# Kernel tuning notes

Measured on AMD Instinct MI355X. Metric: run time of the kernel, lower is better.

The kernel has to match this reference:

```python
import jax, jax.numpy as jnp
import numpy as np

N_NODES = 100000
N_EDGES = 1600000
N_PAIRS = 500000
K_HOPS = 6


def _bn(x, g, b, eps):
    # training-mode batch norm over the node/edge (batch) axis, biased variance
    mu = jnp.mean(x, axis=0)
    var = jnp.var(x, axis=0)
    return (x - mu) * jax.lax.rsqrt(var + eps) * g + b


def _gelu(x):
    return jax.nn.gelu(x, approximate=False)  # torch GELU default (erf)


def setup_inputs() -> dict:
    key = jax.random.key(0)
    ks = jax.random.split(key, 20)
    F, EF = 128, 32

    def w(k, shape, s=0.05):
        return jax.random.normal(k, shape, dtype=jnp.float32) * s

    return {
        'X': jax.random.normal(ks[0], (N_NODES, F), jnp.float32),
        'Y': jax.random.normal(ks[1], (N_PAIRS, EF), jnp.float32),
        'edge_index': jax.random.randint(ks[2], (2, N_EDGES), 0, N_NODES, jnp.int32),
        'inds0': jax.random.randint(ks[3], (N_PAIRS,), 0, N_NODES, jnp.int32),
        'inds1': jax.random.randint(ks[4], (N_PAIRS,), 0, N_NODES, jnp.int32),
        'bn_node_g': jnp.ones((F,), jnp.float32),
        'bn_node_b': jnp.zeros((F,), jnp.float32),
        'tag_lin_W': w(ks[5], (F, 128)),
        'tag_lin_b': jnp.zeros((128,), jnp.float32),
        'tag_Ws': w(ks[6], (K_HOPS + 1, 128, 128)),
        'tag_bias': jnp.zeros((128,), jnp.float32),
        'nl_W0': w(ks[7], (256, 256)),
        'nl_b0': jnp.zeros((256,), jnp.float32),
        'nl_W1': w(ks[8], (256, 128)),
        'nl_b1': jnp.zeros((128,), jnp.float32),
        'cl_W': w(ks[9], (128, 128)),
        'cl_b': jnp.zeros((128,), jnp.float32),
        'end_W': w(ks[10], (128, 8)),
        'end_b': jnp.zeros((8,), jnp.float32),
        'bn_edge_g': jnp.ones((544,), jnp.float32),
        'bn_edge_b': jnp.zeros((544,), jnp.float32),
        'el_W0': w(ks[11], (544, 512)),
        'el_b0': jnp.zeros((512,), jnp.float32),
        'el_W1': w(ks[12], (512, 256)),
        'el_b1': jnp.zeros((256,), jnp.float32),
        'el_end_W': w(ks[13], (256, 1)),
        'el_end_b': jnp.zeros((1,), jnp.float32),
    }


def reference(X, Y, bn_node_g, bn_node_b, tag_lin_W, tag_lin_b, tag_Ws, tag_bias,
              nl_W0, nl_b0, nl_W1, nl_b1, cl_W, cl_b, end_W, end_b,
              bn_edge_g, bn_edge_b, el_W0, el_b0, el_W1, el_b1, el_end_W, el_end_b,
              edge_index, inds0, inds1):
    N = X.shape[0]
    # ---- NodeGLAM ----
    x = _bn(X, bn_node_g, bn_node_b, 1e-5)
    # TagModule: Linear -> GELU -> TAGConv -> GELU
    h = _gelu(x @ tag_lin_W + tag_lin_b)
    src, dst = edge_index[0], edge_index[1]
    # gcn_norm (no self loops): deg over target, norm = d^-1/2[src]*d^-1/2[dst]
    deg = jax.ops.segment_sum(jnp.ones(src.shape, h.dtype), dst, num_segments=N)
    dinv = jnp.where(deg > 0, jax.lax.rsqrt(jnp.maximum(deg, 1.0)), 0.0)
    wgt = (dinv[src] * dinv[dst])[:, None]  # [E,1]
    out = h @ tag_Ws[0]
    hk = h
    for k in range(1, K_HOPS + 1):
        hk = jax.ops.segment_sum(hk[src] * wgt, dst, num_segments=N)  # gather-scale-scatter
        out = out + hk @ tag_Ws[k]
    h = _gelu(out + tag_bias)
    a = jnp.concatenate([x, h], axis=1)  # [N, 256]
    a = _gelu(a @ nl_W0 + nl_b0)
    a = _gelu(a @ nl_W1 + nl_b1)  # Node_embs [N,128]
    cl = _gelu(a @ cl_W + cl_b)
    node_classes = jax.nn.softmax(cl @ end_W + end_b, axis=-1)  # [N,8]
    # ---- edge feature gather + EdgeGLAM ----
    Omega = jnp.concatenate([a[inds0], a[inds1], X[inds0], X[inds1], Y], axis=1)  # [P,544]
    o = _bn(Omega, bn_edge_g, bn_edge_b, 1.0)  # BatchNorm(input_, output_) -> eps=1
    o = _gelu(o @ el_W0 + el_b0)
    o = _gelu(o @ el_W1 + el_b1)
    e_pred = jax.nn.sigmoid(o @ el_end_W + el_end_b)[:, 0]  # [P]
    return (node_classes, e_pred)
```

## Files before the change

kernel.cpp:

```cpp
#include <hip/hip_runtime.h>
#include <math.h>

#define NN 100000
#define NE 1600000
#define NP 500000
#define KHOPS 6
#define ECHK 75000
#define NB_SCAN ((NN + 1023) / 1024)

typedef unsigned short u16;
typedef short bf16x8 __attribute__((ext_vector_type(8)));
typedef float f32x4 __attribute__((ext_vector_type(4)));

__device__ __forceinline__ float gelu_erf(float x) {
    return 0.5f * x * (1.0f + erff(x * 0.70710678118654752f));
}
__device__ __forceinline__ float b2f(u16 u) {
    return __uint_as_float(((unsigned int)u) << 16);
}
__device__ __forceinline__ u16 f2b(float f) {
    unsigned int x = __float_as_uint(f);
    return (u16)((x + 0x7FFFu + ((x >> 16) & 1u)) >> 16);
}
__device__ __forceinline__ bf16x8 cvt8(float4 a, float4 b) {
    bf16x8 v;
    v[0]=(short)f2b(a.x); v[1]=(short)f2b(a.y); v[2]=(short)f2b(a.z); v[3]=(short)f2b(a.w);
    v[4]=(short)f2b(b.x); v[5]=(short)f2b(b.y); v[6]=(short)f2b(b.z); v[7]=(short)f2b(b.w);
    return v;
}

template<int BF>
__global__ void col_stats(const void* __restrict__ Matv, int rows, int lc,
                          const int* __restrict__ w0, const int* __restrict__ w1,
                          float* __restrict__ sums, float* __restrict__ sumsq,
                          int base0, int base1)
{
    __shared__ float red[256];
    const int t = threadIdx.x;
    const int C = 1 << lc;
    const long total = (long)rows << lc;
    const long stride = (long)gridDim.x * 256;
    float s0 = 0.f, q0 = 0.f, s1 = 0.f, q1 = 0.f;
    for (long idx = (long)blockIdx.x * 256 + t; idx < total; idx += stride) {
        int r = (int)(idx >> lc);
        float v = BF ? b2f(((const u16*)Matv)[idx]) : ((const float*)Matv)[idx];
        float f0 = w0 ? (float)w0[r] : 1.0f;
        s0 += f0 * v;
        q0 += f0 * v * v;
        if (w1) {
            float f1 = (float)w1[r];
            s1 += f1 * v;
            q1 += f1 * v * v;
        }
    }
    red[t] = s0; __syncthreads();
    if (t < C) { float x = 0.f; for (int k = t; k < 256; k += C) x += red[k]; atomicAdd(&sums[base0 + t], x); }
    __syncthreads();
    red[t] = q0; __syncthreads();
    if (t < C) { float x = 0.f; for (int k = t; k < 256; k += C) x += red[k]; atomicAdd(&sumsq[base0 + t], x); }
    __syncthreads();
    if (w1) {
        red[t] = s1; __syncthreads();
        if (t < C) { float x = 0.f; for (int k = t; k < 256; k += C) x += red[k]; atomicAdd(&sums[base1 + t], x); }
        __syncthreads();
        red[t] = q1; __syncthreads();
        if (t < C) { float x = 0.f; for (int k = t; k < 256; k += C) x += red[k]; atomicAdd(&sumsq[base1 + t], x); }
    }
}

__global__ void bn_finalize(const float* __restrict__ sums, const float* __restrict__ sumsq,
                            const float* __restrict__ g, const float* __restrict__ b,
                            float* __restrict__ s, float* __restrict__ t,
                            int C, float count, float eps)
{
    int c = blockIdx.x * blockDim.x + threadIdx.x;
    if (c < C) {
        float mu = sums[c] / count;
        float var = sumsq[c] / count - mu * mu;
        float sc = g[c] * rsqrtf(var + eps);
        s[c] = sc;
        t[c] = b[c] - mu * sc;
    }
}

__global__ void gelu_bias_bf(const float* __restrict__ x, const float* __restrict__ bias,
                             u16* __restrict__ out, int n4)
{
    int stride = gridDim.x * blockDim.x;
    for (int i = blockIdx.x * blockDim.x + threadIdx.x; i < n4; i += stride) {
        int c4 = (i & 31) * 4;
        float4 v = ((const float4*)x)[i];
        ushort4 o;
        o.x = f2b(gelu_erf(v.x + bias[c4 + 0]));
        o.y = f2b(gelu_erf(v.y + bias[c4 + 1]));
        o.z = f2b(gelu_erf(v.z + bias[c4 + 2]));
        o.w = f2b(gelu_erf(v.w + bias[c4 + 3]));
        ((ushort4*)out)[i] = o;
    }
}

__global__ void hist_add(const int* __restrict__ idx, int n, int* __restrict__ cnt)
{
    int stride = gridDim.x * blockDim.x;
    for (int i = blockIdx.x * blockDim.x + threadIdx.x; i < n; i += stride)
        atomicAdd(&cnt[idx[i]], 1);
}

__global__ void hist_add2(const int* __restrict__ i0, const int* __restrict__ i1, int n,
                          int* __restrict__ c0, int* __restrict__ c1)
{
    int stride = gridDim.x * blockDim.x;
    for (int i = blockIdx.x * blockDim.x + threadIdx.x; i < n; i += stride) {
        atomicAdd(&c0[i0[i]], 1);
        atomicAdd(&c1[i1[i]], 1);
    }
}

__global__ void scan1(const int* __restrict__ cnt, int* __restrict__ ex,
                      int* __restrict__ part, int n)
{
    __shared__ int buf[1024];
    int b = blockIdx.x, t = threadIdx.x;
    int i = b * 1024 + t;
    int v = (i < n) ? cnt[i] : 0;
    buf[t] = v;
    __syncthreads();
    int incl = v;
    for (int o = 1; o < 1024; o <<= 1) {
        int tmp = (t >= o) ? buf[t - o] : 0;
        __syncthreads();
        incl += tmp;
        buf[t] = incl;
        __syncthreads();
    }
    if (i < n) ex[i] = incl - v;
    if (t == 1023) part[b] = incl;
}

__global__ void scan2(int* __restrict__ part, int nb)
{
    __shared__ int s[256];
    int t = threadIdx.x;
    if (t < nb) s[t] = part[t];
    __syncthreads();
    if (t == 0) {
        int run = 0;
        for (int b = 0; b < nb; ++b) { int x = s[b]; part[b] = run; run += x; }
        part[nb] = run;
    }
}

__global__ void scan3(int* __restrict__ indptr, const int* __restrict__ part,
                      const int* __restrict__ cnt, float* __restrict__ dinv, int n)
{
    int b = blockIdx.x, t = threadIdx.x;
    int i = b * 1024 + t;
    if (i < n) {
        indptr[i] += part[b];
        int c = cnt[i];
        dinv[i] = (c > 0) ? rsqrtf((float)c) : 0.f;
    }
    if (b == 0 && t == 0) indptr[n] = part[NB_SCAN];
}

__global__ void csr_build(const int* __restrict__ src, const int* __restrict__ dst, int n,
                          const int* __restrict__ indptr, int* __restrict__ cursor,
                          int* __restrict__ csrS)
{
    int stride = gridDim.x * blockDim.x;
    for (int e = blockIdx.x * blockDim.x + threadIdx.x; e < n; e += stride) {
        int s = src[e], d = dst[e];
        int pos = indptr[d] + atomicAdd(&cursor[d], 1);
        __builtin_nontemporal_store(s, &csrS[pos]);
    }
}

__global__ void spmm_hop(const u16* __restrict__ hin, u16* __restrict__ hout,
                         const int* __restrict__ indptr, const int* __restrict__ csrS,
                         const float* __restrict__ dinv)
{
    int gid = blockIdx.x * blockDim.x + threadIdx.x;
    int node = gid >> 6;
    int lane = gid & 63;
    if (node >= NN) return;
    float dn = dinv[node];
    int beg = indptr[node], end = indptr[node + 1];
    float a0 = 0.f, a1 = 0.f;
    int e = beg;
    for (; e + 1 < end; e += 2) {
        int s0 = csrS[e], s1 = csrS[e + 1];
        float w0 = dn * dinv[s0], w1 = dn * dinv[s1];
        ushort2 p0 = *(const ushort2*)(hin + (size_t)s0 * 128 + lane * 2);
        ushort2 p1 = *(const ushort2*)(hin + (size_t)s1 * 128 + lane * 2);
        a0 = fmaf(w0, b2f(p0.x), a0);
        a1 = fmaf(w0, b2f(p0.y), a1);
        a0 = fmaf(w1, b2f(p1.x), a0);
        a1 = fmaf(w1, b2f(p1.y), a1);
    }
    if (e < end) {
        int s0 = csrS[e];
        float w0 = dn * dinv[s0];
        ushort2 p0 = *(const ushort2*)(hin + (size_t)s0 * 128 + lane * 2);
        a0 = fmaf(w0, b2f(p0.x), a0);
        a1 = fmaf(w0, b2f(p0.y), a1);
    }
    ushort2 o;
    o.x = f2b(a0); o.y = f2b(a1);
    *(ushort2*)(hout + (size_t)node * 128 + lane * 2) = o;
}

__global__ void convTB(const float* __restrict__ in, u16* __restrict__ out,
                       int K, int Nc, int B)
{
    int per = K * Nc;
    int i = blockIdx.x * blockDim.x + threadIdx.x;
    if (i < per * B) {
        int m = i / per, r = i - m * per;
        int n = r / K, k = r - n * K;
        out[i] = f2b(in[(size_t)m * per + (size_t)k * Nc + n]);
    }
}

__global__ void fold_wT(const float* __restrict__ W0, const float* __restrict__ s,
                        u16* __restrict__ out)
{
    int i = blockIdx.x * blockDim.x + threadIdx.x;
    if (i < 512 * 544) {
        int n = i / 544, k = i - n * 544;
        out[i] = f2b(s[k] * W0[(size_t)k * 512 + n]);
    }
}

__global__ void fold_b(const float* __restrict__ W0, const float* __restrict__ b0,
                       const float* __restrict__ tv, float* __restrict__ bp)
{
    int j = blockIdx.x * blockDim.x + threadIdx.x;
    if (j < 512) {
        float s = b0[j];
        for (int k = 0; k < 544; ++k) s = fmaf(tv[k], W0[k * 512 + j], s);
        bp[j] = s;
    }
}

template<int AMODE>
__device__ __forceinline__ bf16x8 load_a_slot(
    const void* __restrict__ A0v, const void* __restrict__ A1v,
    const float* __restrict__ Yp, const int* __restrict__ i0s, const int* __restrict__ i1s,
    int rowOffset, const float* __restrict__ sv, const float* __restrict__ tv,
    int row, int r, int k0, int sl, int Mr, int lda)
{
    bf16x8 val = {0, 0, 0, 0, 0, 0, 0, 0};
    if (row < Mr) {
        if (AMODE == 0) {
            val = *(const bf16x8*)((const u16*)A0v + (size_t)row * lda + k0 + sl * 8);
        } else if (AMODE == 1) {
            int c = k0 + sl * 8;
            if (c < 128) {
                const float* xp = (const float*)A0v + (size_t)row * 128 + c;
                float4 x0 = *(const float4*)xp, x1 = *(const float4*)(xp + 4);
                float4 s0 = *(const float4*)(sv + c), s1 = *(const float4*)(sv + c + 4);
                float4 t0 = *(const float4*)(tv + c), t1 = *(const float4*)(tv + c + 4);
                float4 a = make_float4(fmaf(x0.x,s0.x,t0.x), fmaf(x0.y,s0.y,t0.y),
                                       fmaf(x0.z,s0.z,t0.z), fmaf(x0.w,s0.w,t0.w));
                float4 b = make_float4(fmaf(x1.x,s1.x,t1.x), fmaf(x1.y,s1.y,t1.y),
                                       fmaf(x1.z,s1.z,t1.z), fmaf(x1.w,s1.w,t1.w));
                val = cvt8(a, b);
            } else {
                val = *(const bf16x8*)((const u16*)A1v + (size_t)row * 128 + (c - 128));
            }
        } else if (AMODE == 3) {
            int c = k0 + sl * 8;
            const float* xp = (const float*)A0v + (size_t)row * 128 + c;
            float4 x0 = *(const float4*)xp, x1 = *(const float4*)(xp + 4);
            float4 s0 = *(const float4*)(sv + c), s1 = *(const float4*)(sv + c + 4);
            float4 t0 = *(const float4*)(tv + c), t1 = *(const float4*)(tv + c + 4);
            float4 a = make_float4(fmaf(x0.x,s0.x,t0.x), fmaf(x0.y,s0.y,t0.y),
                                   fmaf(x0.z,s0.z,t0.z), fmaf(x0.w,s0.w,t0.w));
            float4 b = make_float4(fmaf(x1.x,s1.x,t1.x), fmaf(x1.y,s1.y,t1.y),
                                   fmaf(x1.z,s1.z,t1.z), fmaf(x1.w,s1.w,t1.w));
            val = cvt8(a, b);
        } else {
            int seg = k0 >> 7;
            int c = (k0 & 127) + sl * 8;
            if (seg == 0) {
                val = *(const bf16x8*)((const u16*)A0v + (size_t)i0s[r] * 128 + c);
            } else if (seg == 1) {
                val = *(const bf16x8*)((const u16*)A0v + (size_t)i1s[r] * 128 + c);
            } else if (seg == 2) {
                const float* xp = (const float*)A1v + (size_t)i0s[r] * 128 + c;
                val = cvt8(*(const float4*)xp, *(const float4*)(xp + 4));
            } else if (seg == 3) {
                const float* xp = (const float*)A1v + (size_t)i1s[r] * 128 + c;
                val = cvt8(*(const float4*)xp, *(const float4*)(xp + 4));
            } else {
                const float* yp = Yp + (size_t)(rowOffset + row) * 32 + sl * 8;
                val = cvt8(*(const float4*)yp, *(const float4*)(yp + 4));
            }
        }
    }
    return val;
}

template<int AMODE, int ACT, int ACCUM, int OUTBF>
__launch_bounds__(256, 2)
__global__ void gemm_mfma(const void* __restrict__ A0v, const void* __restrict__ A1v,
                          const float* __restrict__ Yp,
                          const int* __restrict__ I0, const int* __restrict__ I1,
                          int rowOffset,
                          const float* __restrict__ sv, const float* __restrict__ tv,
                          const u16* __restrict__ Wb, const float* __restrict__ bias,
                          void* __restrict__ Cv, int Mr, int Kd, int Nc, int lda)
{
    __shared__ __align__(16) u16 As[128 * 32];
    __shared__ __align__(16) u16 Bs[128 * 32];
    __shared__ int i0s[128], i1s[128];

    const int t = threadIdx.x;
    const int lane = t & 63;
    const int wid = t >> 6;
    const int wm = wid >> 1, wn = wid & 1;
    const int lb = lane & 15, lh = lane >> 4;
    const int row0 = blockIdx.x * 128;
    const int colb = blockIdx.y * 128;

    if (AMODE == 2) {
        if (t < 128) {
            int r = row0 + t;
            i0s[t] = (r < Mr) ? I0[rowOffset + r] : 0;
        } else {
            int r = row0 + (t - 128);
            i1s[t - 128] = (r < Mr) ? I1[rowOffset + r] : 0;
        }
    }

    f32x4 acc[4][4];
#pragma unroll
    for (int i = 0; i < 4; ++i)
#pragma unroll
        for (int j = 0; j < 4; ++j) acc[i][j] = (f32x4){0.f, 0.f, 0.f, 0.f};

    for (int k0 = 0; k0 < Kd; k0 += 32) {
        __syncthreads();
#pragma unroll
        for (int h = 0; h < 2; ++h) {
            int s = t + h * 256;
            int r = s >> 2, sl = s & 3;
            bf16x8 val = load_a_slot<AMODE>(A0v, A1v, Yp, i0s, i1s, rowOffset, sv, tv,
                                            row0 + r, r, k0, sl, Mr, lda);
            *(bf16x8*)&As[r * 32 + ((sl ^ ((r >> 1) & 3)) << 3)] = val;
        }
#pragma unroll
        for (int h = 0; h < 2; ++h) {
            int s = t + h * 256;
            int n = s >> 2, sl = s & 3;
            bf16x8 val = *(const bf16x8*)(Wb + (size_t)(colb + n) * Kd + k0 + sl * 8);
            *(bf16x8*)&Bs[n * 32 + ((sl ^ ((n >> 1) & 3)) << 3)] = val;
        }
        __syncthreads();
        bf16x8 af[4], bfr[4];
#pragma unroll
        for (int i = 0; i < 4; ++i) {
            int r = wm * 64 + i * 16 + lb;
            af[i] = *(const bf16x8*)&As[r * 32 + ((lh ^ ((r >> 1) & 3)) << 3)];
        }
#pragma unroll
        for (int j = 0; j < 4; ++j) {
            int n = wn * 64 + j * 16 + lb;
            bfr[j] = *(const bf16x8*)&Bs[n * 32 + ((lh ^ ((n >> 1) & 3)) << 3)];
        }
#pragma unroll
        for (int i = 0; i < 4; ++i)
#pragma unroll
            for (int j = 0; j < 4; ++j)
                acc[i][j] = __builtin_amdgcn_mfma_f32_16x16x32_bf16(af[i], bfr[j], acc[i][j], 0, 0, 0);
    }

#pragma unroll
    for (int i = 0; i < 4; ++i) {
#pragma unroll
        for (int j = 0; j < 4; ++j) {
            int col = colb + wn * 64 + j * 16 + lb;
#pragma unroll
            for (int r = 0; r < 4; ++r) {
                int row = row0 + wm * 64 + i * 16 + lh * 4 + r;
                if (row < Mr) {
                    size_t off = (size_t)row * Nc + col;
                    float v = acc[i][j][r];
                    if (ACCUM) v += ((const float*)Cv)[off];
                    if (ACT) v = gelu_erf(v + bias[col]);
                    if (OUTBF) ((u16*)Cv)[off] = f2b(v);
                    else       ((float*)Cv)[off] = v;
                }
            }
        }
    }
}

template<int AMODE, int ACT, int OUTBF>
__launch_bounds__(512, 4)
__global__ void gemm_wide(const void* __restrict__ A0v, const void* __restrict__ A1v,
                          const float* __restrict__ Yp,
                          const int* __restrict__ I0, const int* __restrict__ I1,
                          int rowOffset,
                          const float* __restrict__ sv, const float* __restrict__ tv,
                          const u16* __restrict__ Wb, const float* __restrict__ bias,
                          void* __restrict__ Cv, int Mr, int Kd, int Nc)
{
    __shared__ __align__(16) u16 As[128 * 32];
    __shared__ __align__(16) u16 Bs[256 * 32];
    __shared__ int i0s[128], i1s[128];

    const int t = threadIdx.x;
    const int lane = t & 63;
    const int wid = t >> 6;
    const int wm = wid >> 2, wn = wid & 3;
    const int lb = lane & 15, lh = lane >> 4;
    const int row0 = blockIdx.x * 128;
    const int colb = blockIdx.y * 256;

    if (AMODE == 2) {
        if (t < 128) {
            int r = row0 + t;
            i0s[t] = (r < Mr) ? I0[rowOffset + r] : 0;
        } else if (t < 256) {
            int r = row0 + (t - 128);
            i1s[t - 128] = (r < Mr) ? I1[rowOffset + r] : 0;
        }
    }

    f32x4 acc[4][4];
#pragma unroll
    for (int i = 0; i < 4; ++i)
#pragma unroll
        for (int j = 0; j < 4; ++j) acc[i][j] = (f32x4){0.f, 0.f, 0.f, 0.f};

    for (int k0 = 0; k0 < Kd; k0 += 32) {
        __syncthreads();
        {
            int r = t >> 2, sl = t & 3;
            bf16x8 val = load_a_slot<AMODE>(A0v, A1v, Yp, i0s, i1s, rowOffset, sv, tv,
                                            row0 + r, r, k0, sl, Mr, 0);
            *(bf16x8*)&As[r * 32 + ((sl ^ ((r >> 1) & 3)) << 3)] = val;
        }
#pragma unroll
        for (int h = 0; h < 2; ++h) {
            int s = t + h * 512;
            int n = s >> 2, sl = s & 3;
            bf16x8 val = *(const bf16x8*)(Wb + (size_t)(colb + n) * Kd + k0 + sl * 8);
            *(bf16x8*)&Bs[n * 32 + ((sl ^ ((n >> 1) & 3)) << 3)] = val;
        }
        __syncthreads();
        bf16x8 af[4], bfr[4];
#pragma unroll
        for (int i = 0; i < 4; ++i) {
            int r = wm * 64 + i * 16 + lb;
            af[i] = *(const bf16x8*)&As[r * 32 + ((lh ^ ((r >> 1) & 3)) << 3)];
        }
#pragma unroll
        for (int j = 0; j < 4; ++j) {
            int n = wn * 64 + j * 16 + lb;
            bfr[j] = *(const bf16x8*)&Bs[n * 32 + ((lh ^ ((n >> 1) & 3)) << 3)];
        }
#pragma unroll
        for (int i = 0; i < 4; ++i)
#pragma unroll
            for (int j = 0; j < 4; ++j)
                acc[i][j] = __builtin_amdgcn_mfma_f32_16x16x32_bf16(af[i], bfr[j], acc[i][j], 0, 0, 0);
    }

#pragma unroll
    for (int i = 0; i < 4; ++i) {
#pragma unroll
        for (int j = 0; j < 4; ++j) {
            int col = colb + wn * 64 + j * 16 + lb;
#pragma unroll
            for (int r = 0; r < 4; ++r) {
                int row = row0 + wm * 64 + i * 16 + lh * 4 + r;
                if (row < Mr) {
                    size_t off = (size_t)row * Nc + col;
                    float v = acc[i][j][r];
                    if (ACT) v = gelu_erf(v + bias[col]);
                    if (OUTBF) ((u16*)Cv)[off] = f2b(v);
                    else       ((float*)Cv)[off] = v;
                }
            }
        }
    }
}

__launch_bounds__(512, 4)
__global__ void gemm_head(const u16* __restrict__ A0, const u16* __restrict__ Wb,
                          const float* __restrict__ bias,
                          const float* __restrict__ eW,
                          const float* __restrict__ eb,
                          float* __restrict__ outp, int outOffset, int Mr)
{
    __shared__ __align__(16) u16 As[128 * 32];
    __shared__ __align__(16) u16 Bs[256 * 32];
    __shared__ float bls[256], ews[256];
    __shared__ float sred[4][128];

    const int t = threadIdx.x;
    const int lane = t & 63;
    const int wid = t >> 6;
    const int wm = wid >> 2, wn = wid & 3;
    const int lb = lane & 15, lh = lane >> 4;
    const int row0 = blockIdx.x * 128;
    const int Kd = 512;

    if (t < 256) { bls[t] = bias[t]; ews[t] = eW[t]; }

    f32x4 acc[4][4];
#pragma unroll
    for (int i = 0; i < 4; ++i)
#pragma unroll
        for (int j = 0; j < 4; ++j) acc[i][j] = (f32x4){0.f, 0.f, 0.f, 0.f};

    for (int k0 = 0; k0 < Kd; k0 += 32) {
        __syncthreads();
        {
            int r = t >> 2, sl = t & 3;
            int row = row0 + r;
            bf16x8 val = {0,0,0,0,0,0,0,0};
            if (row < Mr) val = *(const bf16x8*)(A0 + (size_t)row * 512 + k0 + sl * 8);
            *(bf16x8*)&As[r * 32 + ((sl ^ ((r >> 1) & 3)) << 3)] = val;
        }
#pragma unroll
        for (int h = 0; h < 2; ++h) {
            int s = t + h * 512;
            int n = s >> 2, sl = s & 3;
            bf16x8 val = *(const bf16x8*)(Wb + (size_t)n * Kd + k0 + sl * 8);
            *(bf16x8*)&Bs[n * 32 + ((sl ^ ((n >> 1) & 3)) << 3)] = val;
        }
        __syncthreads();
        bf16x8 af[4], bfr[4];
#pragma unroll
        for (int i = 0; i < 4; ++i) {
            int r = wm * 64 + i * 16 + lb;
            af[i] = *(const bf16x8*)&As[r * 32 + ((lh ^ ((r >> 1) & 3)) << 3)];
        }
#pragma unroll
        for (int j = 0; j < 4; ++j) {
            int n = wn * 64 + j * 16 + lb;
            bfr[j] = *(const bf16x8*)&Bs[n * 32 + ((lh ^ ((n >> 1) & 3)) << 3)];
        }
#pragma unroll
        for (int i = 0; i < 4; ++i)
#pragma unroll
            for (int j = 0; j < 4; ++j)
                acc[i][j] = __builtin_amdgcn_mfma_f32_16x16x32_bf16(af[i], bfr[j], acc[i][j], 0, 0, 0);
    }

#pragma unroll
    for (int i = 0; i < 4; ++i) {
#pragma unroll
        for (int r = 0; r < 4; ++r) {
            float p = 0.f;
#pragma unroll
            for (int j = 0; j < 4; ++j) {
                int col = wn * 64 + j * 16 + lb;
                p += gelu_erf(acc[i][j][r] + bls[col]) * ews[col];
            }
            p += __shfl_xor(p, 1);
            p += __shfl_xor(p, 2);
            p += __shfl_xor(p, 4);
            p += __shfl_xor(p, 8);
            if (lb == 0) sred[wn][wm * 64 + i * 16 + lh * 4 + r] = p;
        }
    }
    __syncthreads();
    if (t < 128) {
        int row = row0 + t;
        if (row < Mr) {
            float s = sred[0][t] + sred[1][t] + sred[2][t] + sred[3][t] + eb[0];
            outp[outOffset + row] = 1.f / (1.f + expf(-s));
        }
    }
}

__global__ void node_head(const float* __restrict__ cl, const float* __restrict__ Wend,
                          const float* __restrict__ bend, float* __restrict__ out, int m)
{
    __shared__ float WsT[8 * 128];
    __shared__ float bs[8];
    int t = threadIdx.x;
    for (int i = t; i < 1024; i += 256) {
        int k = i >> 3, j = i & 7;
        WsT[j * 128 + k] = Wend[i];
    }
    if (t < 8) bs[t] = bend[t];
    __syncthreads();
    int gid = blockIdx.x * 256 + t;
    int wave = gid >> 6, lane = gid & 63;
    if (wave >= m) return;
    float v0 = cl[(size_t)wave * 128 + lane];
    float v1 = cl[(size_t)wave * 128 + lane + 64];
    float lg[8];
#pragma unroll
    for (int j = 0; j < 8; ++j) {
        float p = v0 * WsT[j * 128 + lane] + v1 * WsT[j * 128 + lane + 64];
#pragma unroll
        for (int o = 32; o; o >>= 1) p += __shfl_down(p, o);
        lg[j] = p;
    }
    if (lane == 0) {
        float mx = -1e30f;
#pragma unroll
        for (int j = 0; j < 8; ++j) { lg[j] += bs[j]; mx = fmaxf(mx, lg[j]); }
        float s = 0.f;
#pragma unroll
        for (int j = 0; j < 8; ++j) { lg[j] = expf(lg[j] - mx); s += lg[j]; }
        float inv = 1.f / s;
#pragma unroll
        for (int j = 0; j < 8; ++j) out[(size_t)wave * 8 + j] = lg[j] * inv;
    }
}

extern "C" void kernel_launch(void* const* d_in, const int* in_sizes, int n_in,
                              void* d_out, int out_size, void* d_ws, size_t ws_size,
                              hipStream_t stream)
{
    const float* X    = (const float*)d_in[0];
    const float* Y    = (const float*)d_in[1];
    const int*   EI   = (const int*)d_in[2];
    const int*   I0   = (const int*)d_in[3];
    const int*   I1   = (const int*)d_in[4];
    const float* bnG  = (const float*)d_in[5];
    const float* bnB  = (const float*)d_in[6];
    const float* Wlin = (const float*)d_in[7];
    const float* blin = (const float*)d_in[8];
    const float* tagWs= (const float*)d_in[9];
    const float* tagB = (const float*)d_in[10];
    const float* nlW0 = (const float*)d_in[11];
    const float* nlb0 = (const float*)d_in[12];
    const float* nlW1 = (const float*)d_in[13];
    const float* nlb1 = (const float*)d_in[14];
    const float* clW  = (const float*)d_in[15];
    const float* clb  = (const float*)d_in[16];
    const float* endW = (const float*)d_in[17];
    const float* endB = (const float*)d_in[18];
    const float* beG  = (const float*)d_in[19];
    const float* beB  = (const float*)d_in[20];
    const float* elW0 = (const float*)d_in[21];
    const float* elb0 = (const float*)d_in[22];
    const float* elW1 = (const float*)d_in[23];
    const float* elb1 = (const float*)d_in[24];
    const float* elEW = (const float*)d_in[25];
    const float* elEb = (const float*)d_in[26];

    const int N = NN, E = NE, P = NP;

    char* w = (char*)d_ws;
    size_t off = 0;
    auto alloc = [&](size_t bytes) -> void* {
        void* p = w + off;
        off += (bytes + 255) & ~(size_t)255;
        return p;
    };

    size_t zeroBytes = (size_t)(544 + 544 + 128 + 128) * 4 + (size_t)4 * N * 4;
    char* zr = (char*)alloc(zeroBytes);
    float* statS = (float*)zr;
    float* statQ = statS + 544;
    float* nodeS = statQ + 544;
    float* nodeQ = nodeS + 128;
    int* cnt    = (int*)(nodeQ + 128);
    int* cursor = cnt + N;
    int* cnt0   = cursor + N;
    int* cnt1   = cnt0 + N;

    int*   indptr = (int*)alloc((size_t)(N + 1) * 4);
    int*   part   = (int*)alloc((size_t)(NB_SCAN + 1) * 4);
    float* dinv   = (float*)alloc((size_t)N * 4);
    int*   csrS   = (int*)alloc((size_t)E * 4);
    float* sNode  = (float*)alloc(128 * 4);
    float* tNode  = (float*)alloc(128 * 4);
    float* sEdge  = (float*)alloc(544 * 4);
    float* tEdge  = (float*)alloc(544 * 4);
    float* b0p    = (float*)alloc(512 * 4);
    u16* Wlinb  = (u16*)alloc((size_t)128 * 128 * 2);
    u16* tagWsb = (u16*)alloc((size_t)7 * 128 * 128 * 2);
    u16* nlW0b  = (u16*)alloc((size_t)256 * 256 * 2);
    u16* nlW1b  = (u16*)alloc((size_t)128 * 256 * 2);
    u16* clWb   = (u16*)alloc((size_t)128 * 128 * 2);
    u16* elW1b  = (u16*)alloc((size_t)256 * 512 * 2);
    u16* W0pb   = (u16*)alloc((size_t)512 * 544 * 2);
    u16*   hA   = (u16*)alloc((size_t)N * 128 * 2);
    u16*   hB   = (u16*)alloc((size_t)N * 128 * 2);
    float* outT = (float*)alloc((size_t)N * 128 * 4);

    if (ws_size < off) return;

    u16*   aEmb  = hA;
    u16*   houtb = hB;
    float* out_nodes = (float*)d_out;
    float* out_epred = (float*)d_out + (size_t)N * 8;

    hipMemsetAsync(zr, 0, zeroBytes, stream);

    convTB<<<(128*128 + 255)/256, 256, 0, stream>>>(Wlin, Wlinb, 128, 128, 1);
    convTB<<<(7*128*128 + 255)/256, 256, 0, stream>>>(tagWs, tagWsb, 128, 128, 7);
    convTB<<<(256*256 + 255)/256, 256, 0, stream>>>(nlW0, nlW0b, 256, 256, 1);
    convTB<<<(256*128 + 255)/256, 256, 0, stream>>>(nlW1, nlW1b, 256, 128, 1);
    convTB<<<(128*128 + 255)/256, 256, 0, stream>>>(clW, clWb, 128, 128, 1);
    convTB<<<(512*256 + 255)/256, 256, 0, stream>>>(elW1, elW1b, 512, 256, 1);

    col_stats<0><<<1024, 256, 0, stream>>>(X, N, 7, nullptr, nullptr, nodeS, nodeQ, 0, 0);
    bn_finalize<<<1, 128, 0, stream>>>(nodeS, nodeQ, bnG, bnB, sNode, tNode, 128, (float)N, 1e-5f);

    dim3 g1((N + 127) / 128, 1);
    gemm_mfma<3, 1, 0, 1><<<g1, 256, 0, stream>>>(X, nullptr, nullptr, nullptr, nullptr, 0,
                                                  sNode, tNode, Wlinb, blin, hA, N, 128, 128, 128);

    hist_add<<<2048, 256, 0, stream>>>(EI + E, E, cnt);
    hist_add2<<<1024, 256, 0, stream>>>(I0, I1, P, cnt0, cnt1);
    scan1<<<NB_SCAN, 1024, 0, stream>>>(cnt, indptr, part, N);
    scan2<<<1, 256, 0, stream>>>(part, NB_SCAN);
    scan3<<<NB_SCAN, 1024, 0, stream>>>(indptr, part, cnt, dinv, N);
    csr_build<<<2048, 256, 0, stream>>>(EI, EI + E, E, indptr, cursor, csrS);

    gemm_mfma<0, 0, 0, 0><<<g1, 256, 0, stream>>>(hA, nullptr, nullptr, nullptr, nullptr, 0,
                                                  nullptr, nullptr, tagWsb, nullptr, outT, N, 128, 128, 128);
    u16* cur = hA; u16* nxt = hB;
    for (int k = 1; k <= KHOPS; ++k) {
        spmm_hop<<<(N * 64 + 255) / 256, 256, 0, stream>>>(cur, nxt, indptr, csrS, dinv);
        gemm_mfma<0, 0, 1, 0><<<g1, 256, 0, stream>>>(nxt, nullptr, nullptr, nullptr, nullptr, 0,
                                                      nullptr, nullptr, tagWsb + (size_t)k*128*128,
                                                      nullptr, outT, N, 128, 128, 128);
        u16* tmp = cur; cur = nxt; nxt = tmp;
    }
    gelu_bias_bf<<<2048, 256, 0, stream>>>(outT, tagB, houtb, N * 128 / 4);

    u16*   a256  = (u16*)outT;
    float* clbuf = outT;
    {
        dim3 gA((N + 127) / 128, 1);
        gemm_wide<1, 1, 1><<<gA, 512, 0, stream>>>(X, houtb, nullptr, nullptr, nullptr, 0,
                                                   sNode, tNode, nlW0b, nlb0, a256, N, 256, 256);
        dim3 gB((N + 127) / 128, 1);
        gemm_mfma<0, 1, 0, 1><<<gB, 256, 0, stream>>>(a256, nullptr, nullptr, nullptr, nullptr, 0,
                                                      nullptr, nullptr, nlW1b, nlb1, aEmb, N, 256, 128, 256);
        gemm_mfma<0, 1, 0, 0><<<gB, 256, 0, stream>>>(aEmb, nullptr, nullptr, nullptr, nullptr, 0,
                                                      nullptr, nullptr, clWb, clb, clbuf, N, 128, 128, 128);
        node_head<<<(N + 3) / 4, 256, 0, stream>>>(clbuf, endW, endB, out_nodes, N);
    }

    col_stats<1><<<1024, 256, 0, stream>>>(aEmb, N, 7, cnt0, cnt1, statS, statQ, 0, 128);
    col_stats<0><<<1024, 256, 0, stream>>>(X,    N, 7, cnt0, cnt1, statS, statQ, 256, 384);
    col_stats<0><<<1024, 256, 0, stream>>>(Y,    P, 5, nullptr, nullptr, statS, statQ, 512, 0);
    bn_finalize<<<3, 256, 0, stream>>>(statS, statQ, beG, beB, sEdge, tEdge, 544, (float)P, 1.0f);
    fold_wT<<<(512*544 + 255)/256, 256, 0, stream>>>(elW0, sEdge, W0pb);
    fold_b<<<2, 256, 0, stream>>>(elW0, elb0, tEdge, b0p);

    u16* o1 = hB;
    for (int pb = 0; pb < P; pb += ECHK) {
        int m = (P - pb < ECHK) ? (P - pb) : ECHK;
        dim3 gA((m + 127) / 128, 2);
        gemm_wide<2, 1, 1><<<gA, 512, 0, stream>>>(aEmb, X, Y, I0, I1, pb,
                                                   nullptr, nullptr, W0pb, b0p, o1, m, 544, 512);
        dim3 gB((m + 127) / 128, 1);
        gemm_head<<<gB, 512, 0, stream>>>(o1, elW1b, elb1, elEW, elEb, out_epred, pb, m);
    }
}
```

Measured before the change: 2.570 ms.

## Fuse final hop GELU into GEMM, pre-convert X to bf16, unroll SpMM

Several changes at once. The last TAG hop's GEMM now applies bias+GELU and writes bf16 directly, which removes the separate gelu_bias_bf pass over the fp32 accumulator. X is converted to bf16 once, so the edge GEMM gathers bf16 rows of X instead of fp32, and the X column statistics are computed from the bf16 copy. The SpMM inner loop is unrolled by four for more memory-level parallelism, the nontemporal store in the CSR build is dropped, and the edge chunk size is reduced to 50000. Computing the X column statistics from bf16 values changes the batch-norm statistics slightly, and the edge output buffer is moved to outT.

```diff
diff --git a/kernel.cpp b/kernel.cpp
--- a/kernel.cpp
+++ b/kernel.cpp
@@ -5,7 +5,7 @@
 #define NE 1600000
 #define NP 500000
 #define KHOPS 6
-#define ECHK 75000
+#define ECHK 50000
 #define NB_SCAN ((NN + 1023) / 1024)
 
 typedef unsigned short u16;
@@ -83,22 +83,6 @@
     }
 }
 
-__global__ void gelu_bias_bf(const float* __restrict__ x, const float* __restrict__ bias,
-                             u16* __restrict__ out, int n4)
-{
-    int stride = gridDim.x * blockDim.x;
-    for (int i = blockIdx.x * blockDim.x + threadIdx.x; i < n4; i += stride) {
-        int c4 = (i & 31) * 4;
-        float4 v = ((const float4*)x)[i];
-        ushort4 o;
-        o.x = f2b(gelu_erf(v.x + bias[c4 + 0]));
-        o.y = f2b(gelu_erf(v.y + bias[c4 + 1]));
-        o.z = f2b(gelu_erf(v.z + bias[c4 + 2]));
-        o.w = f2b(gelu_erf(v.w + bias[c4 + 3]));
-        ((ushort4*)out)[i] = o;
-    }
-}
-
 __global__ void hist_add(const int* __restrict__ idx, int n, int* __restrict__ cnt)
 {
     int stride = gridDim.x * blockDim.x;
@@ -171,7 +155,7 @@
     for (int e = blockIdx.x * blockDim.x + threadIdx.x; e < n; e += stride) {
         int s = src[e], d = dst[e];
         int pos = indptr[d] + atomicAdd(&cursor[d], 1);
-        __builtin_nontemporal_store(s, &csrS[pos]);
+        csrS[pos] = s;
     }
 }
 
@@ -187,17 +171,20 @@
     int beg = indptr[node], end = indptr[node + 1];
     float a0 = 0.f, a1 = 0.f;
     int e = beg;
-    for (; e + 1 < end; e += 2) {
-        int s0 = csrS[e], s1 = csrS[e + 1];
+    for (; e + 3 < end; e += 4) {
+        int s0 = csrS[e], s1 = csrS[e + 1], s2 = csrS[e + 2], s3 = csrS[e + 3];
         float w0 = dn * dinv[s0], w1 = dn * dinv[s1];
+        float w2 = dn * dinv[s2], w3 = dn * dinv[s3];
         ushort2 p0 = *(const ushort2*)(hin + (size_t)s0 * 128 + lane * 2);
         ushort2 p1 = *(const ushort2*)(hin + (size_t)s1 * 128 + lane * 2);
-        a0 = fmaf(w0, b2f(p0.x), a0);
-        a1 = fmaf(w0, b2f(p0.y), a1);
-        a0 = fmaf(w1, b2f(p1.x), a0);
-        a1 = fmaf(w1, b2f(p1.y), a1);
-    }
-    if (e < end) {
+        ushort2 p2 = *(const ushort2*)(hin + (size_t)s2 * 128 + lane * 2);
+        ushort2 p3 = *(const ushort2*)(hin + (size_t)s3 * 128 + lane * 2);
+        a0 = fmaf(w0, b2f(p0.x), a0); a1 = fmaf(w0, b2f(p0.y), a1);
+        a0 = fmaf(w1, b2f(p1.x), a0); a1 = fmaf(w1, b2f(p1.y), a1);
+        a0 = fmaf(w2, b2f(p2.x), a0); a1 = fmaf(w2, b2f(p2.y), a1);
+        a0 = fmaf(w3, b2f(p3.x), a0); a1 = fmaf(w3, b2f(p3.y), a1);
+    }
+    for (; e < end; ++e) {
         int s0 = csrS[e];
         float w0 = dn * dinv[s0];
         ushort2 p0 = *(const ushort2*)(hin + (size_t)s0 * 128 + lane * 2);
@@ -218,6 +205,17 @@
         int m = i / per, r = i - m * per;
         int n = r / K, k = r - n * K;
         out[i] = f2b(in[(size_t)m * per + (size_t)k * Nc + n]);
+    }
+}
+
+__global__ void convB(const float* __restrict__ in, u16* __restrict__ out, int n4)
+{
+    int stride = gridDim.x * blockDim.x;
+    for (int i = blockIdx.x * blockDim.x + threadIdx.x; i < n4; i += stride) {
+        float4 v = ((const float4*)in)[i];
+        ushort4 o;
+        o.x = f2b(v.x); o.y = f2b(v.y); o.z = f2b(v.z); o.w = f2b(v.w);
+        ((ushort4*)out)[i] = o;
     }
 }
 
@@ -287,11 +285,9 @@
             } else if (seg == 1) {
                 val = *(const bf16x8*)((const u16*)A0v + (size_t)i1s[r] * 128 + c);
             } else if (seg == 2) {
-                const float* xp = (const float*)A1v + (size_t)i0s[r] * 128 + c;
-                val = cvt8(*(const float4*)xp, *(const float4*)(xp + 4));
+                val = *(const bf16x8*)((const u16*)A1v + (size_t)i0s[r] * 128 + c);
             } else if (seg == 3) {
-                const float* xp = (const float*)A1v + (size_t)i1s[r] * 128 + c;
-                val = cvt8(*(const float4*)xp, *(const float4*)(xp + 4));
+                val = *(const bf16x8*)((const u16*)A1v + (size_t)i1s[r] * 128 + c);
             } else {
                 const float* yp = Yp + (size_t)(rowOffset + row) * 32 + sl * 8;
                 val = cvt8(*(const float4*)yp, *(const float4*)(yp + 4));
@@ -309,7 +305,8 @@
                           int rowOffset,
                           const float* __restrict__ sv, const float* __restrict__ tv,
                           const u16* __restrict__ Wb, const float* __restrict__ bias,
-                          void* __restrict__ Cv, int Mr, int Kd, int Nc, int lda)
+                          void* __restrict__ Cv, const float* __restrict__ Cacc,
+                          int Mr, int Kd, int Nc, int lda)
 {
     __shared__ __align__(16) u16 As[128 * 32];
     __shared__ __align__(16) u16 Bs[128 * 32];
@@ -386,7 +383,7 @@
                 if (row < Mr) {
                     size_t off = (size_t)row * Nc + col;
                     float v = acc[i][j][r];
-                    if (ACCUM) v += ((const float*)Cv)[off];
+                    if (ACCUM) v += Cacc[off];
                     if (ACT) v = gelu_erf(v + bias[col]);
                     if (OUTBF) ((u16*)Cv)[off] = f2b(v);
                     else       ((float*)Cv)[off] = v;
@@ -490,8 +487,7 @@
 
 __launch_bounds__(512, 4)
 __global__ void gemm_head(const u16* __restrict__ A0, const u16* __restrict__ Wb,
-                          const float* __restrict__ bias,
-                          const float* __restrict__ eW,
+                          const float* __restrict__ bias, const float* __restrict__ eW,
                           const float* __restrict__ eb,
                           float* __restrict__ outp, int outOffset, int Mr)
 {
@@ -710,7 +706,7 @@
 
     dim3 g1((N + 127) / 128, 1);
     gemm_mfma<3, 1, 0, 1><<<g1, 256, 0, stream>>>(X, nullptr, nullptr, nullptr, nullptr, 0,
-                                                  sNode, tNode, Wlinb, blin, hA, N, 128, 128, 128);
+                                                  sNode, tNode, Wlinb, blin, hA, nullptr, N, 128, 128, 128);
 
     hist_add<<<2048, 256, 0, stream>>>(EI + E, E, cnt);
     hist_add2<<<1024, 256, 0, stream>>>(I0, I1, P, cnt0, cnt1);
@@ -720,16 +716,20 @@
     csr_build<<<2048, 256, 0, stream>>>(EI, EI + E, E, indptr, cursor, csrS);
 
     gemm_mfma<0, 0, 0, 0><<<g1, 256, 0, stream>>>(hA, nullptr, nullptr, nullptr, nullptr, 0,
-                                                  nullptr, nullptr, tagWsb, nullptr, outT, N, 128, 128, 128);
+                                                  nullptr, nullptr, tagWsb, nullptr, outT, nullptr,
+                                                  N, 128, 128, 128);
     u16* cur = hA; u16* nxt = hB;
-    for (int k = 1; k <= KHOPS; ++k) {
+    for (int k = 1; k < KHOPS; ++k) {
         spmm_hop<<<(N * 64 + 255) / 256, 256, 0, stream>>>(cur, nxt, indptr, csrS, dinv);
         gemm_mfma<0, 0, 1, 0><<<g1, 256, 0, stream>>>(nxt, nullptr, nullptr, nullptr, nullptr, 0,
                                                       nullptr, nullptr, tagWsb + (size_t)k*128*128,
-                                                      nullptr, outT, N, 128, 128, 128);
+                                                      nullptr, outT, outT, N, 128, 128, 128);
         u16* tmp = cur; cur = nxt; nxt = tmp;
     }
-    gelu_bias_bf<<<2048, 256, 0, stream>>>(outT, tagB, houtb, N * 128 / 4);
+    spmm_hop<<<(N * 64 + 255) / 256, 256, 0, stream>>>(cur, nxt, indptr, csrS, dinv);
+    gemm_mfma<0, 1, 1, 1><<<g1, 256, 0, stream>>>(nxt, nullptr, nullptr, nullptr, nullptr, 0,
+                                                  nullptr, nullptr, tagWsb + (size_t)KHOPS*128*128,
+                                                  tagB, houtb, outT, N, 128, 128, 128);
 
     u16*   a256  = (u16*)outT;
     float* clbuf = outT;
@@ -739,24 +739,29 @@
                                                    sNode, tNode, nlW0b, nlb0, a256, N, 256, 256);
         dim3 gB((N + 127) / 128, 1);
         gemm_mfma<0, 1, 0, 1><<<gB, 256, 0, stream>>>(a256, nullptr, nullptr, nullptr, nullptr, 0,
-                                                      nullptr, nullptr, nlW1b, nlb1, aEmb, N, 256, 128, 256);
+                                                      nullptr, nullptr, nlW1b, nlb1, aEmb, nullptr,
+                                                      N, 256, 128, 256);
         gemm_mfma<0, 1, 0, 0><<<gB, 256, 0, stream>>>(aEmb, nullptr, nullptr, nullptr, nullptr, 0,
-                                                      nullptr, nullptr, clWb, clb, clbuf, N, 128, 128, 128);
+                                                      nullptr, nullptr, clWb, clb, clbuf, nullptr,
+                                                      N, 128, 128, 128);
         node_head<<<(N + 3) / 4, 256, 0, stream>>>(clbuf, endW, endB, out_nodes, N);
     }
 
+    u16* Xb = hB;
+    convB<<<2048, 256, 0, stream>>>(X, Xb, N * 128 / 4);
+
     col_stats<1><<<1024, 256, 0, stream>>>(aEmb, N, 7, cnt0, cnt1, statS, statQ, 0, 128);
-    col_stats<0><<<1024, 256, 0, stream>>>(X,    N, 7, cnt0, cnt1, statS, statQ, 256, 384);
+    col_stats<1><<<1024, 256, 0, stream>>>(Xb,   N, 7, cnt0, cnt1, statS, statQ, 256, 384);
     col_stats<0><<<1024, 256, 0, stream>>>(Y,    P, 5, nullptr, nullptr, statS, statQ, 512, 0);
     bn_finalize<<<3, 256, 0, stream>>>(statS, statQ, beG, beB, sEdge, tEdge, 544, (float)P, 1.0f);
     fold_wT<<<(512*544 + 255)/256, 256, 0, stream>>>(elW0, sEdge, W0pb);
     fold_b<<<2, 256, 0, stream>>>(elW0, elb0, tEdge, b0p);
 
-    u16* o1 = hB;
+    u16* o1 = (u16*)outT;
     for (int pb = 0; pb < P; pb += ECHK) {
         int m = (P - pb < ECHK) ? (P - pb) : ECHK;
         dim3 gA((m + 127) / 128, 2);
-        gemm_wide<2, 1, 1><<<gA, 512, 0, stream>>>(aEmb, X, Y, I0, I1, pb,
+        gemm_wide<2, 1, 1><<<gA, 512, 0, stream>>>(aEmb, Xb, Y, I0, I1, pb,
                                                    nullptr, nullptr, W0pb, b0p, o1, m, 544, 512);
         dim3 gB((m + 127) / 128, 1);
         gemm_head<<<gB, 512, 0, stream>>>(o1, elW1b, elb1, elEW, elEb, out_epred, pb, m);
```

Result: faster. 2.339 ms (-9.0%).
